# Performance work log

Measured on AMD Instinct MI355X. Metric: run time of the kernel, lower is better.

## Reference

```python
import jax, jax.numpy as jnp
import numpy as np

MODEL_DIM = 1024
NUM_HEADS = 16
D_K = MODEL_DIM // NUM_HEADS  # 64
MAX_SEQ_LEN = 3200
B, T = 2, 2048
THETA_BASE = 10000.0


def setup_inputs() -> dict:
    key = jax.random.key(0)
    ks = jax.random.split(key, 5)
    scale = 1.0 / np.sqrt(MODEL_DIM)
    x = jax.random.normal(ks[0], (B, T, MODEL_DIM), dtype=jnp.float32)
    wq = jax.random.normal(ks[1], (MODEL_DIM, MODEL_DIM), dtype=jnp.float32) * scale
    wk = jax.random.normal(ks[2], (MODEL_DIM, MODEL_DIM), dtype=jnp.float32) * scale
    wv = jax.random.normal(ks[3], (MODEL_DIM, MODEL_DIM), dtype=jnp.float32) * scale
    wo = jax.random.normal(ks[4], (MODEL_DIM, MODEL_DIM), dtype=jnp.float32) * scale
    bq = jnp.zeros((MODEL_DIM,), jnp.float32)
    bk = jnp.zeros((MODEL_DIM,), jnp.float32)
    bv = jnp.zeros((MODEL_DIM,), jnp.float32)
    bo = jnp.zeros((MODEL_DIM,), jnp.float32)
    # RoPE tables, exactly as precompute_rotation_matrix: theta duplicated
    # adjacently ([t0,t0,t1,t1,...]).
    theta = THETA_BASE ** (jnp.arange(D_K // 2, dtype=jnp.float32) * (-2.0 / D_K))
    ang = jnp.outer(jnp.arange(MAX_SEQ_LEN, dtype=jnp.float32), theta)  # [L, d/2]
    ang = jnp.repeat(ang, 2, axis=-1)  # [L, d]
    return {
        "x": x, "wq": wq, "bq": bq, "wk": wk, "bk": bk,
        "wv": wv, "bv": bv, "wo": wo, "bo": bo,
        "cos": jnp.cos(ang), "sin": jnp.sin(ang),
    }


def reference(x, wq, bq, wk, bk, wv, bv, wo, bo, cos, sin):
    b, t, dm = x.shape
    h, d = NUM_HEADS, dm // NUM_HEADS

    # NOTE: original uses .view(b, h, t, d) directly on [b, t, h*d] (no
    # transpose) — a nonstandard head split we replicate faithfully.
    xq = (x @ wq.T + bq).reshape(b, h, t, d)
    xk = (x @ wk.T + bk).reshape(b, h, t, d)
    xv = (x @ wv.T + bv).reshape(b, h, t, d)

    def rot_half(q):
        # pairs are adjacent (2i, 2i+1): out[2i] = -q[2i+1], out[2i+1] = q[2i]
        q2 = q.reshape(b, h, t, d // 2, 2)
        return jnp.stack([-q2[..., 1], q2[..., 0]], axis=-1).reshape(b, h, t, d)

    # NOTE: original indexes cos/sin at the single position `seq_len`
    # (rotation_matrix_cos[:, :, xq.shape[2], :]), broadcasting one row over
    # all positions — replicated faithfully.
    c = cos[t]  # [d]
    s = sin[t]  # [d]
    xq = xq * c + rot_half(xq) * s
    xk = xk * c + rot_half(xk) * s

    scores = jnp.einsum("bhqd,bhkd->bhqk", xq, xk) / np.sqrt(d)
    p = jax.nn.softmax(scores, axis=-1)  # mask='none', dropout=0.0
    o = jnp.einsum("bhqk,bhkd->bhqd", p, xv)
    o = o.transpose(0, 2, 1, 3).reshape(b, t, dm)  # 'b h t d -> b t (h d)'
    return o @ wo.T + bo
```

## Files before the change

kernel.cpp:

```cpp
#include <hip/hip_runtime.h>

typedef _Float16 half8 __attribute__((ext_vector_type(8)));
typedef _Float16 half4 __attribute__((ext_vector_type(4)));
typedef __fp16 pkh2 __attribute__((ext_vector_type(2)));
typedef float floatx4 __attribute__((ext_vector_type(4)));

#define AS1 __attribute__((address_space(1)))
#define AS3 __attribute__((address_space(3)))


__global__ __launch_bounds__(256) void convert_kernel(
    const float* __restrict__ x, const float* __restrict__ wq,
    const float* __restrict__ wk, const float* __restrict__ wv,
    const float* __restrict__ wo,
    _Float16* __restrict__ xb, _Float16* __restrict__ wqkv,
    _Float16* __restrict__ wob)
{
    int i = (blockIdx.x * 256 + threadIdx.x) * 4;
    const float* src; _Float16* dst; int off;
    if (i < 4194304)      { src = x;  dst = xb;            off = i; }
    else if (i < 5242880) { src = wq; dst = wqkv;          off = i - 4194304; }
    else if (i < 6291456) { src = wk; dst = wqkv + 1048576; off = i - 5242880; }
    else if (i < 7340032) { src = wv; dst = wqkv + 2097152; off = i - 6291456; }
    else                  { src = wo; dst = wob;           off = i - 7340032; }
    float4 v = *(const float4*)(src + off);
    union { uint2 u; pkh2 h[2]; } o;
    o.h[0] = __builtin_amdgcn_cvt_pkrtz(v.x, v.y);
    o.h[1] = __builtin_amdgcn_cvt_pkrtz(v.z, v.w);
    *(uint2*)(dst + off) = o.u;
}

template<bool QKV>
__global__ __launch_bounds__(256) void gemm_kernel(
    const _Float16* __restrict__ A, const _Float16* __restrict__ W,
    const float* __restrict__ b0, const float* __restrict__ b1,
    const float* __restrict__ b2,
    const float* __restrict__ cosr, const float* __restrict__ sinr,
    _Float16* __restrict__ O0, _Float16* __restrict__ O1,
    _Float16* __restrict__ O2, float* __restrict__ Of)
{
    __shared__ __align__(16) _Float16 As[128 * 64];
    __shared__ __align__(16) _Float16 Bs[128 * 64];
    const int tid  = threadIdx.x;
    const int lane = tid & 63, w = tid >> 6;
    const int lrow = lane & 15, quad = lane >> 4;
    const int wr = (w & 1) * 64, wc = (w >> 1) * 64;
    const int arow0 = blockIdx.x * 128;
    const int brow0 = blockIdx.y * 128;

    const int r8 = lane >> 3;
    const int gcol = ((lane & 7) ^ r8) * 8;

    floatx4 acc[4][4] = {};

    for (int kk = 0; kk < 1024; kk += 64) {
        __syncthreads();
        for (int u = 0; u < 4; u++) {
            const int row = w * 32 + u * 8;
            __builtin_amdgcn_global_load_lds(
                (const AS1 unsigned*)(const void*)(A + (size_t)(arow0 + row + r8) * 1024 + kk + gcol),
                (AS3 unsigned*)(void*)(As + row * 64), 16, 0, 0);
            __builtin_amdgcn_global_load_lds(
                (const AS1 unsigned*)(const void*)(W + (size_t)(brow0 + row + r8) * 1024 + kk + gcol),
                (AS3 unsigned*)(void*)(Bs + row * 64), 16, 0, 0);
        }
        __syncthreads();
        for (int ks = 0; ks < 2; ks++) {
            const int swz = ((ks * 4 + quad) ^ (lrow & 7)) * 8;
            half8 af[4], bf[4];
            for (int mt = 0; mt < 4; mt++)
                af[mt] = *(const half8*)&As[(wr + mt * 16 + lrow) * 64 + swz];
            for (int nt = 0; nt < 4; nt++)
                bf[nt] = *(const half8*)&Bs[(wc + nt * 16 + lrow) * 64 + swz];
            for (int mt = 0; mt < 4; mt++)
                for (int nt = 0; nt < 4; nt++)
                    acc[mt][nt] = __builtin_amdgcn_mfma_f32_16x16x32_f16(
                        af[mt], bf[nt], acc[mt][nt], 0, 0, 0);
        }
    }

    if (QKV) {
        const int seg = blockIdx.y >> 3;
        const float* bias = seg == 0 ? b0 : (seg == 1 ? b1 : b2);
        _Float16* out = seg == 0 ? O0 : (seg == 1 ? O1 : O2);
        const int nbase = (blockIdx.y & 7) * 128 + wc;
        for (int nt = 0; nt < 4; nt++) {
            const int n = nbase + nt * 16 + lrow;
            const float bv = bias[n];
            const int dj = n & 63;
            const float cv = cosr[dj], sv = sinr[dj];
            const bool odd = (n & 1) != 0;
            for (int mt = 0; mt < 4; mt++)
                for (int r = 0; r < 4; r++) {
                    float v = acc[mt][nt][r] + bv;
                    if (seg < 2) {
                        float p = __shfl_xor(v, 1, 64);
                        v = odd ? (v * cv + p * sv) : (v * cv - p * sv);
                    }
                    if (seg == 0) v *= 0.125f;
                    int row = arow0 + wr + mt * 16 + quad * 4 + r;
                    out[row * 1024 + n] = (_Float16)v;
                }
        }
    } else {
        const int nbase = blockIdx.y * 128 + wc;
        for (int nt = 0; nt < 4; nt++) {
            const int n = nbase + nt * 16 + lrow;
            const float bv = b0[n];
            for (int mt = 0; mt < 4; mt++)
                for (int r = 0; r < 4; r++) {
                    int row = arow0 + wr + mt * 16 + quad * 4 + r;
                    Of[row * 1024 + n] = acc[mt][nt][r] + bv;
                }
        }
    }
}

__global__ __launch_bounds__(256) void vtrans_kernel(
    const _Float16* __restrict__ V, _Float16* __restrict__ VT)
{
    __shared__ __align__(16) _Float16 T[64][72];
    const int tid = threadIdx.x;
    const int kt = blockIdx.x;
    const int bh = blockIdx.y;
    const int bi = bh >> 4, hi = bh & 15;
    const _Float16* Vh = V + (size_t)(bi * 2048 + hi * 128) * 1024 + kt * 4096;
    const int srow = tid >> 3, sblk = tid & 7;
    union { uint4 u; _Float16 h[8]; } a, b;
    a.u = *(const uint4*)(Vh + (2 * srow) * 64 + sblk * 8);
    b.u = *(const uint4*)(Vh + (2 * srow + 1) * 64 + sblk * 8);
    for (int j = 0; j < 8; j++) {
        union { unsigned u; _Float16 h[2]; } pk;
        pk.h[0] = a.h[j]; pk.h[1] = b.h[j];
        *(unsigned*)&T[sblk * 8 + j][2 * srow] = pk.u;
    }
    __syncthreads();
    const int d = tid >> 2, c = tid & 3;
    _Float16* out = VT + ((size_t)bh * 64 + d) * 2048 + kt * 64 + c * 16;
    *(uint4*)(out)     = *(const uint4*)&T[d][c * 16];
    *(uint4*)(out + 8) = *(const uint4*)&T[d][c * 16 + 8];
}

__global__ __launch_bounds__(512, 4) void attn_kernel(
    const _Float16* __restrict__ Q, const _Float16* __restrict__ K,
    const _Float16* __restrict__ VT, _Float16* __restrict__ O)
{
    __shared__ __align__(16) _Float16 Ks[2][2][64][72];
    __shared__ __align__(16) _Float16 Vts[2][2][64][72];

    const int tid  = threadIdx.x;
    const int g    = tid >> 8;
    const int t8   = tid & 255;
    const int lane = tid & 63, w = (tid >> 6) & 3;
    const int lrow = lane & 15, quad = lane >> 4;

    const int bid = blockIdx.x;
    const int bh  = (bid & 7) * 4 + (bid >> 7);
    const int qt  = (bid >> 3) & 15;
    const int bi = bh >> 4, hi = bh & 15;
    const size_t base = (size_t)(bi * 2048 + hi * 128) * 1024;
    const _Float16* Qh  = Q + base;
    const _Float16* Kh  = K + base + (size_t)g * 65536;
    const _Float16* VTh = VT + (size_t)bh * 131072 + g * 1024;

    half8 qf[2][2];
    for (int nt = 0; nt < 2; nt++)
        for (int ks = 0; ks < 2; ks++)
            qf[nt][ks] = *(const half8*)(Qh + (qt * 128 + w * 32 + nt * 16 + lrow) * 64
                                          + ks * 32 + quad * 8);

    floatx4 oacc[4][2] = {};
    float lsum0 = 0.0f, lsum1 = 0.0f;

    const int srow = t8 >> 3, sblk = t8 & 7;
    const int vd = t8 >> 2, vc = t8 & 3;
    const _Float16* vbase = VTh + (size_t)vd * 2048 + vc * 16;

    {
        *(uint4*)&Ks[g][0][srow][sblk * 8]      = *(const uint4*)(Kh + srow * 64 + sblk * 8);
        *(uint4*)&Ks[g][0][srow + 32][sblk * 8] = *(const uint4*)(Kh + (srow + 32) * 64 + sblk * 8);
        *(uint4*)&Vts[g][0][vd][vc * 16]     = *(const uint4*)(vbase);
        *(uint4*)&Vts[g][0][vd][vc * 16 + 8] = *(const uint4*)(vbase + 8);
    }
    __syncthreads();

    const float LOG2E = 1.44269504f;
    const float OFF   = -8.65617025f;

    for (int ktl = 0; ktl < 16; ktl++) {
        const int cur = ktl & 1;
        uint4 k0, k1, v0, v1;
        if (ktl < 15) {
            const _Float16* Kt = Kh + (ktl + 1) * 4096;
            const _Float16* Vt = vbase + (ktl + 1) * 64;
            k0 = *(const uint4*)(Kt + srow * 64 + sblk * 8);
            k1 = *(const uint4*)(Kt + (srow + 32) * 64 + sblk * 8);
            v0 = *(const uint4*)(Vt);
            v1 = *(const uint4*)(Vt + 8);
        }
        for (int kt4 = 0; kt4 < 4; kt4++) {
            floatx4 s0 = {}, s1 = {};
            for (int ks = 0; ks < 2; ks++) {
                half8 af = *(const half8*)&Ks[g][cur][kt4 * 16 + lrow][ks * 32 + quad * 8];
                s0 = __builtin_amdgcn_mfma_f32_16x16x32_f16(af, qf[0][ks], s0, 0, 0, 0);
                s1 = __builtin_amdgcn_mfma_f32_16x16x32_f16(af, qf[1][ks], s1, 0, 0, 0);
            }
            float p00 = __builtin_amdgcn_exp2f(fmaf(s0[0], LOG2E, OFF));
            float p01 = __builtin_amdgcn_exp2f(fmaf(s0[1], LOG2E, OFF));
            float p02 = __builtin_amdgcn_exp2f(fmaf(s0[2], LOG2E, OFF));
            float p03 = __builtin_amdgcn_exp2f(fmaf(s0[3], LOG2E, OFF));
            float p10 = __builtin_amdgcn_exp2f(fmaf(s1[0], LOG2E, OFF));
            float p11 = __builtin_amdgcn_exp2f(fmaf(s1[1], LOG2E, OFF));
            float p12 = __builtin_amdgcn_exp2f(fmaf(s1[2], LOG2E, OFF));
            float p13 = __builtin_amdgcn_exp2f(fmaf(s1[3], LOG2E, OFF));
            lsum0 += (p00 + p01) + (p02 + p03);
            lsum1 += (p10 + p11) + (p12 + p13);
            union { half4 h4; pkh2 h2[2]; } pk0, pk1;
            pk0.h2[0] = __builtin_amdgcn_cvt_pkrtz(p00, p01);
            pk0.h2[1] = __builtin_amdgcn_cvt_pkrtz(p02, p03);
            pk1.h2[0] = __builtin_amdgcn_cvt_pkrtz(p10, p11);
            pk1.h2[1] = __builtin_amdgcn_cvt_pkrtz(p12, p13);
            for (int dt = 0; dt < 4; dt++) {
                half4 av = *(const half4*)&Vts[g][cur][dt * 16 + lrow][kt4 * 16 + quad * 4];
                oacc[dt][0] = __builtin_amdgcn_mfma_f32_16x16x16f16(av, pk0.h4, oacc[dt][0], 0, 0, 0);
                oacc[dt][1] = __builtin_amdgcn_mfma_f32_16x16x16f16(av, pk1.h4, oacc[dt][1], 0, 0, 0);
            }
        }
        if (ktl < 15) {
            const int nxt = cur ^ 1;
            *(uint4*)&Ks[g][nxt][srow][sblk * 8]      = k0;
            *(uint4*)&Ks[g][nxt][srow + 32][sblk * 8] = k1;
            *(uint4*)&Vts[g][nxt][vd][vc * 16]     = v0;
            *(uint4*)&Vts[g][nxt][vd][vc * 16 + 8] = v1;
        }
        __syncthreads();
    }

    float* X = (float*)&Ks[0][0][0][0];
    float* L = (float*)&Vts[1][0][0][0];
    if (g == 1) {
        for (int dt = 0; dt < 4; dt++)
            for (int nt = 0; nt < 2; nt++)
                *(floatx4*)&X[((dt * 2 + nt) * 256 + w * 64 + lane) * 4] = oacc[dt][nt];
        L[(w * 64 + lane) * 2]     = lsum0;
        L[(w * 64 + lane) * 2 + 1] = lsum1;
    }
    __syncthreads();
    if (g == 0) {
        for (int dt = 0; dt < 4; dt++)
            for (int nt = 0; nt < 2; nt++)
                oacc[dt][nt] += *(const floatx4*)&X[((dt * 2 + nt) * 256 + w * 64 + lane) * 4];
        lsum0 += L[(w * 64 + lane) * 2];
        lsum1 += L[(w * 64 + lane) * 2 + 1];
        lsum0 += __shfl_xor(lsum0, 16, 64); lsum0 += __shfl_xor(lsum0, 32, 64);
        lsum1 += __shfl_xor(lsum1, 16, 64); lsum1 += __shfl_xor(lsum1, 32, 64);
        const float inv0 = 1.0f / lsum0, inv1 = 1.0f / lsum1;
        _Float16* Es = &Vts[0][0][0][0] + w * 2304;
        for (int dt = 0; dt < 4; dt++) {
            union { uint2 u; pkh2 h2[2]; } a0, a1;
            a0.h2[0] = __builtin_amdgcn_cvt_pkrtz(oacc[dt][0][0] * inv0, oacc[dt][0][1] * inv0);
            a0.h2[1] = __builtin_amdgcn_cvt_pkrtz(oacc[dt][0][2] * inv0, oacc[dt][0][3] * inv0);
            a1.h2[0] = __builtin_amdgcn_cvt_pkrtz(oacc[dt][1][0] * inv1, oacc[dt][1][1] * inv1);
            a1.h2[1] = __builtin_amdgcn_cvt_pkrtz(oacc[dt][1][2] * inv1, oacc[dt][1][3] * inv1);
            *(uint2*)&Es[lrow * 72 + dt * 16 + quad * 4]        = a0.u;
            *(uint2*)&Es[(16 + lrow) * 72 + dt * 16 + quad * 4] = a1.u;
        }
        const int rw = lane >> 1, hf = lane & 1;
        const size_t orow = (size_t)(bi * 2048 + qt * 128 + w * 32 + rw) * 1024
                            + hi * 64 + hf * 32;
        for (int i = 0; i < 4; i++)
            *(uint4*)(O + orow + i * 8) = *(const uint4*)&Es[rw * 72 + hf * 32 + i * 8];
    }
}

extern "C" void kernel_launch(void* const* d_in, const int* in_sizes, int n_in,
                              void* d_out, int out_size, void* d_ws, size_t ws_size,
                              hipStream_t stream) {
    const float* x    = (const float*)d_in[0];
    const float* wq   = (const float*)d_in[1];
    const float* bq   = (const float*)d_in[2];
    const float* wk   = (const float*)d_in[3];
    const float* bk   = (const float*)d_in[4];
    const float* wv   = (const float*)d_in[5];
    const float* bv   = (const float*)d_in[6];
    const float* wo   = (const float*)d_in[7];
    const float* bo   = (const float*)d_in[8];
    const float* cosT = (const float*)d_in[9];
    const float* sinT = (const float*)d_in[10];

    _Float16* ws   = (_Float16*)d_ws;
    _Float16* xb   = ws;
    _Float16* wqkv = xb + 4194304;
    _Float16* wob  = wqkv + 3145728;
    _Float16* Qb   = wob + 1048576;
    _Float16* Kb   = Qb + 4194304;
    _Float16* Vb   = Kb + 4194304;
    _Float16* Ob   = Vb + 4194304;
    _Float16* VTb  = xb;

    convert_kernel<<<8192, 256, 0, stream>>>(x, wq, wk, wv, wo, xb, wqkv, wob);
    gemm_kernel<true><<<dim3(32, 24), 256, 0, stream>>>(
        xb, wqkv, bq, bk, bv, cosT + 2048 * 64, sinT + 2048 * 64,
        Qb, Kb, Vb, nullptr);
    vtrans_kernel<<<dim3(32, 32), 256, 0, stream>>>(Vb, VTb);
    attn_kernel<<<dim3(512), 512, 0, stream>>>(Qb, Kb, VTb, Ob);
    gemm_kernel<false><<<dim3(32, 8), 256, 0, stream>>>(
        Ob, wob, bo, nullptr, nullptr, nullptr, nullptr,
        nullptr, nullptr, nullptr, (float*)d_out);
}
```

Baseline: 226.0 us.

## Swizzle K/VT global layout, single-buffer LDS, and use 16x16x32 MFMA for PV

The QKV epilogue writes K in an XOR-swizzled column order, and the V transpose writes VT rows swizzled the same way. This lets the attention kernel store tiles into unpadded 64-wide LDS rows without bank conflicts. The attention kernel drops the double-buffered padded LDS for a single buffer with register prefetch and two barriers per tile. It also stages P through a per-wave LDS scratch so the PV product can use the wider 16x16x32 MFMA instead of 16x16x16. The cost is an extra LDS round trip for P and an extra barrier per iteration, traded for less LDS use and fewer MFMA issues.

```diff
diff --git a/kernel.cpp b/kernel.cpp
--- a/kernel.cpp
+++ b/kernel.cpp
@@ -1,7 +1,6 @@
 #include <hip/hip_runtime.h>
 
 typedef _Float16 half8 __attribute__((ext_vector_type(8)));
-typedef _Float16 half4 __attribute__((ext_vector_type(4)));
 typedef __fp16 pkh2 __attribute__((ext_vector_type(2)));
 typedef float floatx4 __attribute__((ext_vector_type(4)));
 
@@ -90,6 +89,9 @@
             const int dj = n & 63;
             const float cv = cosr[dj], sv = sinr[dj];
             const bool odd = (n & 1) != 0;
+            const int ns = (seg == 1)
+                ? ((n & ~56) | ((((n >> 3) ^ (n >> 6)) & 7) << 3))
+                : n;
             for (int mt = 0; mt < 4; mt++)
                 for (int r = 0; r < 4; r++) {
                     float v = acc[mt][nt][r] + bv;
@@ -99,7 +101,7 @@
                     }
                     if (seg == 0) v *= 0.125f;
                     int row = arow0 + wr + mt * 16 + quad * 4 + r;
-                    out[row * 1024 + n] = (_Float16)v;
+                    out[row * 1024 + ns] = (_Float16)v;
                 }
         }
     } else {
@@ -136,22 +138,24 @@
     }
     __syncthreads();
     const int d = tid >> 2, c = tid & 3;
-    _Float16* out = VT + ((size_t)bh * 64 + d) * 2048 + kt * 64 + c * 16;
-    *(uint4*)(out)     = *(const uint4*)&T[d][c * 16];
-    *(uint4*)(out + 8) = *(const uint4*)&T[d][c * 16 + 8];
+    const int xr = d & 7;
+    _Float16* outrow = VT + ((size_t)bh * 64 + d) * 2048 + kt * 64;
+    *(uint4*)(outrow + ((2 * c)     ^ xr) * 8) = *(const uint4*)&T[d][c * 16];
+    *(uint4*)(outrow + ((2 * c + 1) ^ xr) * 8) = *(const uint4*)&T[d][c * 16 + 8];
 }
 
 __global__ __launch_bounds__(512, 4) void attn_kernel(
     const _Float16* __restrict__ Q, const _Float16* __restrict__ K,
     const _Float16* __restrict__ VT, _Float16* __restrict__ O)
 {
-    __shared__ __align__(16) _Float16 Ks[2][2][64][72];
-    __shared__ __align__(16) _Float16 Vts[2][2][64][72];
+    __shared__ __align__(16) _Float16 smem[26624];
 
     const int tid  = threadIdx.x;
     const int g    = tid >> 8;
     const int t8   = tid & 255;
-    const int lane = tid & 63, w = (tid >> 6) & 3;
+    const int wg   = tid >> 6;
+    const int w    = wg & 3;
+    const int lane = tid & 63;
     const int lrow = lane & 15, quad = lane >> 4;
 
     const int bid = blockIdx.x;
@@ -163,6 +167,10 @@
     const _Float16* Kh  = K + base + (size_t)g * 65536;
     const _Float16* VTh = VT + (size_t)bh * 131072 + g * 1024;
 
+    _Float16* Ksg  = smem + g * 4096;
+    _Float16* Vtsg = smem + 8192 + g * 4096;
+    _Float16* Ptw  = smem + 16384 + wg * 1280;
+
     half8 qf[2][2];
     for (int nt = 0; nt < 2; nt++)
         for (int ks = 0; ks < 2; ks++)
@@ -173,71 +181,76 @@
     float lsum0 = 0.0f, lsum1 = 0.0f;
 
     const int srow = t8 >> 3, sblk = t8 & 7;
-    const int vd = t8 >> 2, vc = t8 & 3;
-    const _Float16* vbase = VTh + (size_t)vd * 2048 + vc * 16;
-
-    {
-        *(uint4*)&Ks[g][0][srow][sblk * 8]      = *(const uint4*)(Kh + srow * 64 + sblk * 8);
-        *(uint4*)&Ks[g][0][srow + 32][sblk * 8] = *(const uint4*)(Kh + (srow + 32) * 64 + sblk * 8);
-        *(uint4*)&Vts[g][0][vd][vc * 16]     = *(const uint4*)(vbase);
-        *(uint4*)&Vts[g][0][vd][vc * 16 + 8] = *(const uint4*)(vbase + 8);
-    }
-    __syncthreads();
+    const int vd = t8 >> 2;
+    const int vq0 = (2 * (t8 & 3)) ^ (vd & 7);
+    const int vq1 = vq0 ^ 1;
+    const _Float16* vrow = VTh + (size_t)vd * 2048;
+
+    uint4 k0 = *(const uint4*)(Kh + srow * 64 + sblk * 8);
+    uint4 k1 = *(const uint4*)(Kh + (srow + 32) * 64 + sblk * 8);
+    uint4 v0 = *(const uint4*)(vrow + vq0 * 8);
+    uint4 v1 = *(const uint4*)(vrow + vq1 * 8);
 
     const float LOG2E = 1.44269504f;
     const float OFF   = -8.65617025f;
 
     for (int ktl = 0; ktl < 16; ktl++) {
-        const int cur = ktl & 1;
-        uint4 k0, k1, v0, v1;
+        __syncthreads();
+        *(uint4*)&Ksg[srow * 64 + sblk * 8]        = k0;
+        *(uint4*)&Ksg[(srow + 32) * 64 + sblk * 8] = k1;
+        *(uint4*)&Vtsg[vd * 64 + vq0 * 8] = v0;
+        *(uint4*)&Vtsg[vd * 64 + vq1 * 8] = v1;
         if (ktl < 15) {
             const _Float16* Kt = Kh + (ktl + 1) * 4096;
-            const _Float16* Vt = vbase + (ktl + 1) * 64;
             k0 = *(const uint4*)(Kt + srow * 64 + sblk * 8);
             k1 = *(const uint4*)(Kt + (srow + 32) * 64 + sblk * 8);
-            v0 = *(const uint4*)(Vt);
-            v1 = *(const uint4*)(Vt + 8);
-        }
-        for (int kt4 = 0; kt4 < 4; kt4++) {
-            floatx4 s0 = {}, s1 = {};
-            for (int ks = 0; ks < 2; ks++) {
-                half8 af = *(const half8*)&Ks[g][cur][kt4 * 16 + lrow][ks * 32 + quad * 8];
-                s0 = __builtin_amdgcn_mfma_f32_16x16x32_f16(af, qf[0][ks], s0, 0, 0, 0);
-                s1 = __builtin_amdgcn_mfma_f32_16x16x32_f16(af, qf[1][ks], s1, 0, 0, 0);
+            const _Float16* Vt = vrow + (ktl + 1) * 64;
+            v0 = *(const uint4*)(Vt + vq0 * 8);
+            v1 = *(const uint4*)(Vt + vq1 * 8);
+        }
+        __syncthreads();
+        for (int h = 0; h < 2; h++) {
+            for (int k2 = 0; k2 < 2; k2++) {
+                const int kt4 = h * 2 + k2;
+                floatx4 s0 = {}, s1 = {};
+                for (int ks = 0; ks < 2; ks++) {
+                    half8 af = *(const half8*)&Ksg[(kt4 * 16 + lrow) * 64
+                                 + (((ks * 4 + quad) ^ (lrow & 7)) * 8)];
+                    s0 = __builtin_amdgcn_mfma_f32_16x16x32_f16(af, qf[0][ks], s0, 0, 0, 0);
+                    s1 = __builtin_amdgcn_mfma_f32_16x16x32_f16(af, qf[1][ks], s1, 0, 0, 0);
+                }
+                float p00 = __builtin_amdgcn_exp2f(fmaf(s0[0], LOG2E, OFF));
+                float p01 = __builtin_amdgcn_exp2f(fmaf(s0[1], LOG2E, OFF));
+                float p02 = __builtin_amdgcn_exp2f(fmaf(s0[2], LOG2E, OFF));
+                float p03 = __builtin_amdgcn_exp2f(fmaf(s0[3], LOG2E, OFF));
+                float p10 = __builtin_amdgcn_exp2f(fmaf(s1[0], LOG2E, OFF));
+                float p11 = __builtin_amdgcn_exp2f(fmaf(s1[1], LOG2E, OFF));
+                float p12 = __builtin_amdgcn_exp2f(fmaf(s1[2], LOG2E, OFF));
+                float p13 = __builtin_amdgcn_exp2f(fmaf(s1[3], LOG2E, OFF));
+                lsum0 += (p00 + p01) + (p02 + p03);
+                lsum1 += (p10 + p11) + (p12 + p13);
+                union { uint2 u; pkh2 h2[2]; } pk0, pk1;
+                pk0.h2[0] = __builtin_amdgcn_cvt_pkrtz(p00, p01);
+                pk0.h2[1] = __builtin_amdgcn_cvt_pkrtz(p02, p03);
+                pk1.h2[0] = __builtin_amdgcn_cvt_pkrtz(p10, p11);
+                pk1.h2[1] = __builtin_amdgcn_cvt_pkrtz(p12, p13);
+                *(uint2*)&Ptw[lrow * 40 + k2 * 16 + quad * 4]        = pk0.u;
+                *(uint2*)&Ptw[(16 + lrow) * 40 + k2 * 16 + quad * 4] = pk1.u;
             }
-            float p00 = __builtin_amdgcn_exp2f(fmaf(s0[0], LOG2E, OFF));
-            float p01 = __builtin_amdgcn_exp2f(fmaf(s0[1], LOG2E, OFF));
-            float p02 = __builtin_amdgcn_exp2f(fmaf(s0[2], LOG2E, OFF));
-            float p03 = __builtin_amdgcn_exp2f(fmaf(s0[3], LOG2E, OFF));
-            float p10 = __builtin_amdgcn_exp2f(fmaf(s1[0], LOG2E, OFF));
-            float p11 = __builtin_amdgcn_exp2f(fmaf(s1[1], LOG2E, OFF));
-            float p12 = __builtin_amdgcn_exp2f(fmaf(s1[2], LOG2E, OFF));
-            float p13 = __builtin_amdgcn_exp2f(fmaf(s1[3], LOG2E, OFF));
-            lsum0 += (p00 + p01) + (p02 + p03);
-            lsum1 += (p10 + p11) + (p12 + p13);
-            union { half4 h4; pkh2 h2[2]; } pk0, pk1;
-            pk0.h2[0] = __builtin_amdgcn_cvt_pkrtz(p00, p01);
-            pk0.h2[1] = __builtin_amdgcn_cvt_pkrtz(p02, p03);
-            pk1.h2[0] = __builtin_amdgcn_cvt_pkrtz(p10, p11);
-            pk1.h2[1] = __builtin_amdgcn_cvt_pkrtz(p12, p13);
+            half8 bf0 = *(const half8*)&Ptw[lrow * 40 + quad * 8];
+            half8 bf1 = *(const half8*)&Ptw[(16 + lrow) * 40 + quad * 8];
             for (int dt = 0; dt < 4; dt++) {
-                half4 av = *(const half4*)&Vts[g][cur][dt * 16 + lrow][kt4 * 16 + quad * 4];
-                oacc[dt][0] = __builtin_amdgcn_mfma_f32_16x16x16f16(av, pk0.h4, oacc[dt][0], 0, 0, 0);
-                oacc[dt][1] = __builtin_amdgcn_mfma_f32_16x16x16f16(av, pk1.h4, oacc[dt][1], 0, 0, 0);
+                half8 av = *(const half8*)&Vtsg[(dt * 16 + lrow) * 64
+                              + (((h * 4 + quad) ^ (lrow & 7)) * 8)];
+                oacc[dt][0] = __builtin_amdgcn_mfma_f32_16x16x32_f16(av, bf0, oacc[dt][0], 0, 0, 0);
+                oacc[dt][1] = __builtin_amdgcn_mfma_f32_16x16x32_f16(av, bf1, oacc[dt][1], 0, 0, 0);
             }
         }
-        if (ktl < 15) {
-            const int nxt = cur ^ 1;
-            *(uint4*)&Ks[g][nxt][srow][sblk * 8]      = k0;
-            *(uint4*)&Ks[g][nxt][srow + 32][sblk * 8] = k1;
-            *(uint4*)&Vts[g][nxt][vd][vc * 16]     = v0;
-            *(uint4*)&Vts[g][nxt][vd][vc * 16 + 8] = v1;
-        }
-        __syncthreads();
-    }
-
-    float* X = (float*)&Ks[0][0][0][0];
-    float* L = (float*)&Vts[1][0][0][0];
+    }
+    __syncthreads();
+
+    float* X = (float*)smem;
+    float* L = (float*)(smem + 16384);
     if (g == 1) {
         for (int dt = 0; dt < 4; dt++)
             for (int nt = 0; nt < 2; nt++)
@@ -255,7 +268,7 @@
         lsum0 += __shfl_xor(lsum0, 16, 64); lsum0 += __shfl_xor(lsum0, 32, 64);
         lsum1 += __shfl_xor(lsum1, 16, 64); lsum1 += __shfl_xor(lsum1, 32, 64);
         const float inv0 = 1.0f / lsum0, inv1 = 1.0f / lsum1;
-        _Float16* Es = &Vts[0][0][0][0] + w * 2304;
+        _Float16* Es = smem + 17408 + w * 2304;
         for (int dt = 0; dt < 4; dt++) {
             union { uint2 u; pkh2 h2[2]; } a0, a1;
             a0.h2[0] = __builtin_amdgcn_cvt_pkrtz(oacc[dt][0][0] * inv0, oacc[dt][0][1] * inv0);
```

Result: faster. 214.4 us (-5.2%).
